# Kernel optimization log

Measured on AMD Instinct MI355X. Metric: run time of the kernel, lower is better.

The kernel has to match this reference:

```python
import jax, jax.numpy as jnp
import numpy as np

B, D, W = 2048, 512, 512
DEPTH = 6
N_BINS = 2 ** DEPTH          # 64 leaves
N_NODES = 2 ** DEPTH - 1     # 63 inner nodes


def build_indices(depth: int) -> np.ndarray:
    """Root-to-leaf path index table into hstack([probs, 1-probs]).
    Index j selects probs[:, j]; index j + N selects 1 - probs[:, j]."""
    n = 2 ** depth - 1
    paths = []
    for b in range(2 ** depth):
        node, path = 0, []
        for level in range(depth):
            bit = (b >> (depth - 1 - level)) & 1
            path.append(node if bit == 0 else node + n)
            node = 2 * node + 1 + bit
        paths.append(path)
    return np.asarray(paths, dtype=np.int32)  # [2**depth, depth]


def setup_inputs() -> dict:
    key = jax.random.key(0)
    k1, k2, k3, k4 = jax.random.split(key, 4)
    x = jax.random.normal(k1, (B, D), dtype=jnp.float32)
    ray = jax.random.normal(k2, (1, D), dtype=jnp.float32)  # kaiming-normal init
    w_i = jnp.zeros((1, N_NODES), dtype=jnp.float32)
    b_i = jax.random.normal(k3, (1, N_NODES), dtype=jnp.float32)
    a_i = 5.0 * jnp.ones((1, N_NODES), dtype=jnp.float32)
    # kaiming-normal over fan_in = input_width
    inner_transforms = jax.random.normal(k4, (N_BINS, D, W), dtype=jnp.float32) * np.float32((2.0 / D) ** 0.5)
    idx = jnp.asarray(build_indices(DEPTH))  # [64, 6] int32
    return {"x": x, "ray": ray, "w_i": w_i, "b_i": b_i, "a_i": a_i,
            "inner_transforms": inner_transforms, "idx": idx}


def reference(x, ray, w_i, b_i, a_i, inner_transforms, idx):
    eps = 1e-8
    # angles: arccos(cosine_similarity(x, ray)) / pi  -> [B]
    xn = jnp.maximum(jnp.linalg.norm(x, axis=1), eps)
    rn = jnp.maximum(jnp.linalg.norm(ray, axis=1), eps)  # [1]
    cos = (x @ ray[0]) / (xn * rn)
    angles = jnp.arccos(cos) / jnp.pi  # [B]
    # per-node decision probabilities: [B, N_NODES]
    node_fns = (0.5 + jax.nn.sigmoid(w_i)) * angles[:, None] - jax.nn.sigmoid(b_i)
    decisions = jax.nn.sigmoid(node_fns * (1.0 + a_i))
    # tree-indexed gather + product over path -> soft bin distribution [B, N_BINS]
    stacked = jnp.concatenate([decisions, 1.0 - decisions], axis=1)  # [B, 2N]
    bins, depth = idx.shape
    gathered = stacked[:, idx.reshape(-1)].reshape(x.shape[0], bins, depth)
    distribution = jnp.prod(gathered, axis=2)  # [B, L]
    # per-bin linear transforms, weighted by the distribution
    inner = jnp.einsum('bi,liw->blw', x, inner_transforms)  # [B, L, W]
    return jnp.einsum('bl,blo->bo', distribution, inner)  # [B, W]
```

## Files before the change

### kernel.cpp

```cpp
#include <hip/hip_runtime.h>
#include <math.h>

typedef float  f32x4  __attribute__((ext_vector_type(4)));
typedef float  f32x2  __attribute__((ext_vector_type(2)));
typedef short  bf16x8 __attribute__((ext_vector_type(8)));
typedef unsigned short u16x8 __attribute__((ext_vector_type(8)));
typedef unsigned short u16x4 __attribute__((ext_vector_type(4)));

#define B_ROWS 2048
#define D_DIM  512
#define W_DIM  512
#define N_NODES 63
#define N_BINS  64
#define K_TOT   32768
#define NSPLIT  8
#define LPS     (N_BINS / NSPLIT)
#define DEPS    1e-12f

__device__ __forceinline__ unsigned short f2bf(float f) {
    union { float f; unsigned int u; } v; v.f = f;
    unsigned int u = v.u;
    return (unsigned short)((u + 0x7fffu + ((u >> 16) & 1u)) >> 16);
}

__device__ __forceinline__ float sigmoidf_(float z) {
    return 1.0f / (1.0f + expf(-z));
}

__device__ __forceinline__ void load_lds16(const void* g, void* l) {
    __builtin_amdgcn_global_load_lds(
        (const __attribute__((address_space(1))) unsigned int*)g,
        (__attribute__((address_space(3))) unsigned int*)l,
        16, 0, 0);
}

__global__ __launch_bounds__(256) void k_pre(
    const float* __restrict__ x, const float* __restrict__ ray,
    const float* __restrict__ w_i, const float* __restrict__ b_i,
    const float* __restrict__ a_i, const int* __restrict__ idx,
    const float* __restrict__ T,
    float* __restrict__ dist, unsigned short* __restrict__ xb,
    unsigned short* __restrict__ Tt)
{
    __shared__ float tile[64][65];
    const int bid = blockIdx.x;
    const int t   = threadIdx.x;

    if (bid < 4096) {
        const int i0 = (bid & 7) * 64;
        const int w0 = ((bid >> 3) & 7) * 64;
        const int l  = bid >> 6;

        const int w4 = (t & 15) * 4;
        const int ir = t >> 4;
        const float* src = T + ((size_t)(l * 512 + i0)) * 512 + w0;
#pragma unroll
        for (int p = 0; p < 4; ++p) {
            int i = ir + p * 16;
            f32x4 v = *(const f32x4*)(src + (size_t)i * 512 + w4);
            tile[i][w4 + 0] = v.x; tile[i][w4 + 1] = v.y;
            tile[i][w4 + 2] = v.z; tile[i][w4 + 3] = v.w;
        }
        __syncthreads();
#pragma unroll
        for (int rep = 0; rep < 2; ++rep) {
            int id = t + rep * 256;
            int w  = id >> 3;
            int c  = id & 7;
            u16x8 o;
#pragma unroll
            for (int j = 0; j < 8; ++j) o[j] = f2bf(tile[c * 8 + j][w]);
            *(u16x8*)(Tt + (size_t)(w0 + w) * K_TOT + l * 512 + i0 + c * 8) = o;
        }
        return;
    }

    const int pb   = bid - 4096;
    const int wid  = t >> 6;
    const int lane = t & 63;
    const int row  = pb * 4 + wid;
    const float* xr = x + (size_t)row * D_DIM;

    float dotv = 0.f, xx = 0.f, rr = 0.f;
#pragma unroll
    for (int j = 0; j < 2; ++j) {
        f32x4 xv = *(const f32x4*)(xr  + j * 256 + lane * 4);
        f32x4 rv = *(const f32x4*)(ray + j * 256 + lane * 4);
        dotv += xv.x * rv.x + xv.y * rv.y + xv.z * rv.z + xv.w * rv.w;
        xx   += xv.x * xv.x + xv.y * xv.y + xv.z * xv.z + xv.w * xv.w;
        rr   += rv.x * rv.x + rv.y * rv.y + rv.z * rv.z + rv.w * rv.w;
        u16x4 o;
        o[0] = f2bf(xv.x); o[1] = f2bf(xv.y); o[2] = f2bf(xv.z); o[3] = f2bf(xv.w);
        *(u16x4*)(xb + (size_t)row * D_DIM + j * 256 + lane * 4) = o;
    }
#pragma unroll
    for (int off = 1; off < 64; off <<= 1) {
        dotv += __shfl_xor(dotv, off, 64);
        xx   += __shfl_xor(xx,   off, 64);
        rr   += __shfl_xor(rr,   off, 64);
    }
    float xn = fmaxf(sqrtf(xx), 1e-8f);
    float rn = fmaxf(sqrtf(rr), 1e-8f);
    float cosv = dotv / (xn * rn);
    cosv = fminf(1.f, fmaxf(-1.f, cosv));
    float angle = acosf(cosv) * 0.31830988618379067f;

    float dec = 0.f;
    if (lane < N_NODES) {
        float sw = sigmoidf_(w_i[lane]);
        float sb = sigmoidf_(b_i[lane]);
        float nf = (0.5f + sw) * angle - sb;
        dec = sigmoidf_(nf * (1.0f + a_i[lane]));
    }

    float p = 1.f;
#pragma unroll
    for (int v = 0; v < 6; ++v) {
        int j = idx[lane * 6 + v];
        int node = (j < N_NODES) ? j : j - N_NODES;
        float d = __shfl(dec, node, 64);
        p *= (j < N_NODES) ? d : (1.0f - d);
    }
    dist[(size_t)row * N_BINS + lane] = p;
}

__global__ __launch_bounds__(256, 2) void k_gemm9(
    const unsigned short* __restrict__ xb, const unsigned short* __restrict__ Tt,
    const float* __restrict__ dist, float* __restrict__ part)
{
    __shared__ unsigned short As[2][128 * 64];
    __shared__ unsigned short Bs[2][128 * 64];

    const int b   = blockIdx.x;
    const int xcd = b & 7;
    const int j   = b >> 3;
    const int combo = xcd * 4 + (j >> 4);
    const int mblk  = j & 15;
    const int bm0 = mblk * 128;
    const int bn0 = (combo & 3) * 128;
    const int z   = combo >> 2;
    const int l0  = z * LPS;

    const int t    = threadIdx.x;
    const int lane = t & 63;
    const int wid  = t >> 6;
    const int wm = wid >> 1, wn = wid & 1;
    const int lq = lane >> 4, lr = lane & 15;

    const int srow = t >> 3;
    const int c    = t & 7;

    f32x4 acc[4][4];
#pragma unroll
    for (int a = 0; a < 4; ++a)
#pragma unroll
        for (int bb = 0; bb < 4; ++bb)
            acc[a][bb] = (f32x4){0.f, 0.f, 0.f, 0.f};

    const int NIT = LPS * 8;

#define STAGE(it_, buf_)                                                      \
    {                                                                         \
        const int l_  = l0 + ((it_) >> 3);                                    \
        const int i0_ = ((it_) & 7) * 64;                                     \
        _Pragma("unroll")                                                     \
        for (int jj = 0; jj < 4; ++jj) {                                      \
            int row = srow + jj * 32;                                         \
            int cg_ = c ^ (row & 7);                                          \
            load_lds16(xb + (size_t)(bm0 + row) * D_DIM + i0_ + cg_ * 8,      \
                       &As[buf_][row * 64 + c * 8]);                          \
            load_lds16(Tt + (size_t)(bn0 + row) * K_TOT + (size_t)l_ * 512    \
                           + i0_ + cg_ * 8,                                   \
                       &Bs[buf_][row * 64 + c * 8]);                          \
        }                                                                     \
    }

    STAGE(0, 0);

    for (int it = 0; it < NIT; ++it) {
        __syncthreads();
        if (it + 1 < NIT) STAGE(it + 1, (it + 1) & 1);

        if ((it & 7) == 0 && it > 0) {
            const int l = l0 + (it >> 3);
#pragma unroll
            for (int fm = 0; fm < 4; ++fm)
#pragma unroll
                for (int r = 0; r < 4; ++r) {
                    int m = bm0 + wm * 64 + fm * 16 + lq * 4 + r;
                    f32x2 dd = *(const f32x2*)(dist + (size_t)m * N_BINS + (l - 1));
                    float dp = fmaxf(dd.x, DEPS);
                    float dn = fmaxf(dd.y, DEPS);
                    float ratio = dp * __builtin_amdgcn_rcpf(dn);
#pragma unroll
                    for (int fn = 0; fn < 4; ++fn)
                        acc[fm][fn][r] *= ratio;
                }
        }

        const int buf = it & 1;
#pragma unroll
        for (int ks = 0; ks < 2; ++ks) {
            bf16x8 af[4], bfr[4];
#pragma unroll
            for (int fm = 0; fm < 4; ++fm) {
                int m = wm * 64 + fm * 16 + lr;
                int g = ks * 4 + lq;
                af[fm] = *(const bf16x8*)&As[buf][m * 64 + ((g ^ (m & 7)) * 8)];
            }
#pragma unroll
            for (int fn = 0; fn < 4; ++fn) {
                int n = wn * 64 + fn * 16 + lr;
                int g = ks * 4 + lq;
                bfr[fn] = *(const bf16x8*)&Bs[buf][n * 64 + ((g ^ (n & 7)) * 8)];
            }
#pragma unroll
            for (int fm = 0; fm < 4; ++fm)
#pragma unroll
                for (int fn = 0; fn < 4; ++fn)
                    acc[fm][fn] = __builtin_amdgcn_mfma_f32_16x16x32_bf16(
                        af[fm], bfr[fn], acc[fm][fn], 0, 0, 0);
        }
    }

    float* Cp = part + (size_t)z * (B_ROWS * W_DIM);
#pragma unroll
    for (int fm = 0; fm < 4; ++fm)
#pragma unroll
        for (int r = 0; r < 4; ++r) {
            int m = bm0 + wm * 64 + fm * 16 + lq * 4 + r;
            float dl = fmaxf(dist[(size_t)m * N_BINS + (l0 + LPS - 1)], DEPS);
#pragma unroll
            for (int fn = 0; fn < 4; ++fn) {
                int col = bn0 + wn * 64 + fn * 16 + lr;
                Cp[(size_t)m * W_DIM + col] = acc[fm][fn][r] * dl;
            }
        }
#undef STAGE
}

__global__ __launch_bounds__(256) void k_reduce(
    const float* __restrict__ part, float* __restrict__ out, int nsplit)
{
    int i = (blockIdx.x * 256 + threadIdx.x) * 4;
    f32x4 s = *(const f32x4*)(part + i);
    for (int p = 1; p < nsplit; ++p)
        s += *(const f32x4*)(part + (size_t)p * (B_ROWS * W_DIM) + i);
    *(f32x4*)(out + i) = s;
}

__global__ __launch_bounds__(256, 2) void k_gemm_bt(
    const float* __restrict__ x, const float* __restrict__ dist,
    const unsigned short* __restrict__ Tt, float* __restrict__ part,
    int kchunk)
{
    __shared__ unsigned short As[128][72];
    __shared__ unsigned short Bs[128][64];

    const int bm0 = blockIdx.x * 128;
    const int bn0 = blockIdx.y * 128;
    const int kbase = blockIdx.z * kchunk;

    const int lane = threadIdx.x & 63;
    const int wid  = threadIdx.x >> 6;
    const int wm = wid >> 1, wn = wid & 1;
    const int lq = lane >> 4, lr = lane & 15;

    f32x4 acc[4][4];
#pragma unroll
    for (int a = 0; a < 4; ++a)
#pragma unroll
        for (int b = 0; b < 4; ++b)
            acc[a][b] = (f32x4){0.f, 0.f, 0.f, 0.f};

    const int iters = kchunk / 64;
    for (int it = 0; it < iters; ++it) {
        const int k0 = kbase + it * 64;
        const int l  = k0 >> 9;
        const int i0 = k0 & 511;
#pragma unroll
        for (int r2 = 0; r2 < 8; ++r2) {
            int id = threadIdx.x + r2 * 256;
            int m  = id >> 4;
            int kc = id & 15;
            float sc = dist[(size_t)(bm0 + m) * N_BINS + l];
            f32x4 v = *(const f32x4*)(x + (size_t)(bm0 + m) * D_DIM + i0 + kc * 4);
            v *= sc;
            unsigned int p0 = (unsigned int)f2bf(v.x) | ((unsigned int)f2bf(v.y) << 16);
            unsigned int p1 = (unsigned int)f2bf(v.z) | ((unsigned int)f2bf(v.w) << 16);
            unsigned int* dp = (unsigned int*)&As[m][kc * 4];
            dp[0] = p0; dp[1] = p1;
        }
#pragma unroll
        for (int r2 = 0; r2 < 4; ++r2) {
            int id = threadIdx.x + r2 * 256;
            int n  = id >> 3;
            int cc = id & 7;
            int cg = cc ^ (n & 7);
            const u16x8 v = *(const u16x8*)(Tt + (size_t)(bn0 + n) * K_TOT + k0 + cg * 8);
            *(u16x8*)&Bs[n][cc * 8] = v;
        }
        __syncthreads();
#pragma unroll
        for (int ks = 0; ks < 2; ++ks) {
            bf16x8 af[4], bfr[4];
#pragma unroll
            for (int fm = 0; fm < 4; ++fm)
                af[fm] = *(const bf16x8*)&As[wm * 64 + fm * 16 + lr][ks * 32 + lq * 8];
#pragma unroll
            for (int fn = 0; fn < 4; ++fn) {
                int nl = wn * 64 + fn * 16 + lr;
                int cs = (ks * 4 + lq) ^ (nl & 7);
                bfr[fn] = *(const bf16x8*)&Bs[nl][cs * 8];
            }
#pragma unroll
            for (int fm = 0; fm < 4; ++fm)
#pragma unroll
                for (int fn = 0; fn < 4; ++fn)
                    acc[fm][fn] = __builtin_amdgcn_mfma_f32_16x16x32_bf16(
                        af[fm], bfr[fn], acc[fm][fn], 0, 0, 0);
        }
        __syncthreads();
    }

    float* Cp = part + (size_t)blockIdx.z * (B_ROWS * W_DIM);
#pragma unroll
    for (int fm = 0; fm < 4; ++fm)
#pragma unroll
        for (int fn = 0; fn < 4; ++fn)
#pragma unroll
            for (int r = 0; r < 4; ++r) {
                int row = bm0 + wm * 64 + fm * 16 + lq * 4 + r;
                int col = bn0 + wn * 64 + fn * 16 + lr;
                Cp[(size_t)row * W_DIM + col] = acc[fm][fn][r];
            }
}

extern "C" void kernel_launch(void* const* d_in, const int* in_sizes, int n_in,
                              void* d_out, int out_size, void* d_ws, size_t ws_size,
                              hipStream_t stream) {
    const float* x   = (const float*)d_in[0];
    const float* ray = (const float*)d_in[1];
    const float* w_i = (const float*)d_in[2];
    const float* b_i = (const float*)d_in[3];
    const float* a_i = (const float*)d_in[4];
    const float* T   = (const float*)d_in[5];
    const int*   idx = (const int*)d_in[6];
    float* out = (float*)d_out;

    char* ws = (char*)d_ws;
    const size_t distBytes = (size_t)B_ROWS * N_BINS * 4;
    const size_t xbBytes   = (size_t)B_ROWS * D_DIM * 2;
    const size_t ttBytes   = (size_t)W_DIM * K_TOT * 2;
    const size_t partBytes = (size_t)B_ROWS * W_DIM * 4;

    float*          dist = (float*)ws;
    unsigned short* xb   = (unsigned short*)(ws + distBytes);
    unsigned short* Tt   = (unsigned short*)(ws + distBytes + xbBytes);

    if (ws_size >= distBytes + xbBytes + ttBytes + (size_t)NSPLIT * partBytes) {
        float* part = (float*)(ws + distBytes + xbBytes + ttBytes);

        k_pre<<<4096 + 512, 256, 0, stream>>>(x, ray, w_i, b_i, a_i, idx, T,
                                              dist, xb, Tt);
        k_gemm9<<<512, 256, 0, stream>>>(xb, Tt, dist, part);
        k_reduce<<<(B_ROWS * W_DIM) / (256 * 4), 256, 0, stream>>>(part, out, NSPLIT);
    } else if (ws_size >= distBytes + xbBytes + ttBytes) {
        k_pre<<<4096 + 512, 256, 0, stream>>>(x, ray, w_i, b_i, a_i, idx, T,
                                              dist, xb, Tt);
        k_gemm_bt<<<dim3(16, 4, 1), 256, 0, stream>>>(x, dist, Tt, out, K_TOT);
    }
}
```

Before: 192.2 us.

## Use 256x128 tiles with 512 threads and a triple-buffered async prefetch pipeline

The GEMM kernel moves from 128x128 tiles with 256 threads and a double-buffered LDS to 256x128 tiles with 512 threads and three LDS slots. The global-to-LDS loads for the tile two steps ahead are split across the two k-halves and interleaved with the MFMA work, with explicit vmcnt waits, raw s_barrier, and s_setprio around the MFMA blocks. The aim is to hide memory latency better and reuse each loaded B tile across more rows. It uses more LDS and halves the grid to 256 blocks, so occupancy and block scheduling across CUs may change.

```diff
diff --git a/kernel.cpp b/kernel.cpp
--- a/kernel.cpp
+++ b/kernel.cpp
@@ -124,22 +124,19 @@
     dist[(size_t)row * N_BINS + lane] = p;
 }
 
-__global__ __launch_bounds__(256, 2) void k_gemm9(
+__global__ __launch_bounds__(512, 2) void k_gemm10(
     const unsigned short* __restrict__ xb, const unsigned short* __restrict__ Tt,
     const float* __restrict__ dist, float* __restrict__ part)
 {
-    __shared__ unsigned short As[2][128 * 64];
-    __shared__ unsigned short Bs[2][128 * 64];
-
-    const int b   = blockIdx.x;
-    const int xcd = b & 7;
-    const int j   = b >> 3;
-    const int combo = xcd * 4 + (j >> 4);
-    const int mblk  = j & 15;
-    const int bm0 = mblk * 128;
-    const int bn0 = (combo & 3) * 128;
-    const int z   = combo >> 2;
-    const int l0  = z * LPS;
+    __shared__ unsigned short As[3][256 * 64];
+    __shared__ unsigned short Bs[3][128 * 64];
+
+    const int b    = blockIdx.x;
+    const int z    = b & 7;
+    const int tile = b >> 3;
+    const int bm0  = (tile & 7) * 256;
+    const int bn0  = (tile >> 3) * 128;
+    const int l0   = z * LPS;
 
     const int t    = threadIdx.x;
     const int lane = t & 63;
@@ -157,32 +154,38 @@
         for (int bb = 0; bb < 4; ++bb)
             acc[a][bb] = (f32x4){0.f, 0.f, 0.f, 0.f};
 
-    const int NIT = LPS * 8;
-
-#define STAGE(it_, buf_)                                                      \
+#define STAGE_A(u_, slot_, g_)                                                \
     {                                                                         \
-        const int l_  = l0 + ((it_) >> 3);                                    \
-        const int i0_ = ((it_) & 7) * 64;                                     \
-        _Pragma("unroll")                                                     \
-        for (int jj = 0; jj < 4; ++jj) {                                      \
-            int row = srow + jj * 32;                                         \
-            int cg_ = c ^ (row & 7);                                          \
-            load_lds16(xb + (size_t)(bm0 + row) * D_DIM + i0_ + cg_ * 8,      \
-                       &As[buf_][row * 64 + c * 8]);                          \
-            load_lds16(Tt + (size_t)(bn0 + row) * K_TOT + (size_t)l_ * 512    \
-                           + i0_ + cg_ * 8,                                   \
-                       &Bs[buf_][row * 64 + c * 8]);                          \
-        }                                                                     \
-    }
-
-    STAGE(0, 0);
-
-    for (int it = 0; it < NIT; ++it) {
-        __syncthreads();
-        if (it + 1 < NIT) STAGE(it + 1, (it + 1) & 1);
-
-        if ((it & 7) == 0 && it > 0) {
-            const int l = l0 + (it >> 3);
+        const int i0_  = ((u_) & 7) * 64;                                     \
+        const int row_ = srow + (g_) * 64;                                    \
+        const int cg_  = c ^ (row_ & 7);                                      \
+        load_lds16(xb + (size_t)(bm0 + row_) * D_DIM + i0_ + cg_ * 8,         \
+                   &As[slot_][row_ * 64 + c * 8]);                            \
+    }
+#define STAGE_B(u_, slot_, g_)                                                \
+    {                                                                         \
+        const int l_   = l0 + ((u_) >> 3);                                    \
+        const int i0_  = ((u_) & 7) * 64;                                     \
+        const int row_ = srow + (g_) * 64;                                    \
+        const int cg_  = c ^ (row_ & 7);                                      \
+        load_lds16(Tt + (size_t)(bn0 + row_) * K_TOT + (size_t)l_ * 512       \
+                       + i0_ + cg_ * 8,                                       \
+                   &Bs[slot_][row_ * 64 + c * 8]);                            \
+    }
+
+    STAGE_A(0, 0, 0) STAGE_A(0, 0, 1) STAGE_A(0, 0, 2) STAGE_A(0, 0, 3)
+    STAGE_B(0, 0, 0) STAGE_B(0, 0, 1)
+    STAGE_A(1, 1, 0) STAGE_A(1, 1, 1) STAGE_A(1, 1, 2) STAGE_A(1, 1, 3)
+    STAGE_B(1, 1, 0) STAGE_B(1, 1, 1)
+
+    int rs = 0;
+    for (int u = 0; u < 64; ++u) {
+        if (u < 63) asm volatile("s_waitcnt vmcnt(6)" ::: "memory");
+        else        asm volatile("s_waitcnt vmcnt(0)" ::: "memory");
+        __builtin_amdgcn_s_barrier();
+
+        if ((u & 7) == 0 && u > 0) {
+            const int l = l0 + (u >> 3);
 #pragma unroll
             for (int fm = 0; fm < 4; ++fm)
 #pragma unroll
@@ -198,30 +201,59 @@
                 }
         }
 
-        const int buf = it & 1;
-#pragma unroll
-        for (int ks = 0; ks < 2; ++ks) {
-            bf16x8 af[4], bfr[4];
+        const int ws_ = (rs == 0) ? 2 : rs - 1;
+        const bool pf = (u + 2 < 64);
+
+        {
+            bf16x8 af[4], bfv[4];
 #pragma unroll
             for (int fm = 0; fm < 4; ++fm) {
                 int m = wm * 64 + fm * 16 + lr;
-                int g = ks * 4 + lq;
-                af[fm] = *(const bf16x8*)&As[buf][m * 64 + ((g ^ (m & 7)) * 8)];
+                af[fm] = *(const bf16x8*)&As[rs][m * 64 + ((lq ^ (m & 7)) * 8)];
             }
 #pragma unroll
             for (int fn = 0; fn < 4; ++fn) {
                 int n = wn * 64 + fn * 16 + lr;
-                int g = ks * 4 + lq;
-                bfr[fn] = *(const bf16x8*)&Bs[buf][n * 64 + ((g ^ (n & 7)) * 8)];
-            }
+                bfv[fn] = *(const bf16x8*)&Bs[rs][n * 64 + ((lq ^ (n & 7)) * 8)];
+            }
+            if (pf) { STAGE_A(u + 2, ws_, 0) STAGE_A(u + 2, ws_, 1) STAGE_A(u + 2, ws_, 2) }
+            __builtin_amdgcn_s_setprio(1);
 #pragma unroll
             for (int fm = 0; fm < 4; ++fm)
 #pragma unroll
                 for (int fn = 0; fn < 4; ++fn)
                     acc[fm][fn] = __builtin_amdgcn_mfma_f32_16x16x32_bf16(
-                        af[fm], bfr[fn], acc[fm][fn], 0, 0, 0);
-        }
-    }
+                        af[fm], bfv[fn], acc[fm][fn], 0, 0, 0);
+            __builtin_amdgcn_s_setprio(0);
+        }
+        __builtin_amdgcn_s_barrier();
+        {
+            bf16x8 af[4], bfv[4];
+#pragma unroll
+            for (int fm = 0; fm < 4; ++fm) {
+                int m = wm * 64 + fm * 16 + lr;
+                af[fm] = *(const bf16x8*)&As[rs][m * 64 + (((4 + lq) ^ (m & 7)) * 8)];
+            }
+#pragma unroll
+            for (int fn = 0; fn < 4; ++fn) {
+                int n = wn * 64 + fn * 16 + lr;
+                bfv[fn] = *(const bf16x8*)&Bs[rs][n * 64 + (((4 + lq) ^ (n & 7)) * 8)];
+            }
+            if (pf) { STAGE_A(u + 2, ws_, 3) STAGE_B(u + 2, ws_, 0) STAGE_B(u + 2, ws_, 1) }
+            __builtin_amdgcn_s_setprio(1);
+#pragma unroll
+            for (int fm = 0; fm < 4; ++fm)
+#pragma unroll
+                for (int fn = 0; fn < 4; ++fn)
+                    acc[fm][fn] = __builtin_amdgcn_mfma_f32_16x16x32_bf16(
+                        af[fm], bfv[fn], acc[fm][fn], 0, 0, 0);
+            __builtin_amdgcn_s_setprio(0);
+        }
+
+        rs = (rs == 2) ? 0 : rs + 1;
+    }
+#undef STAGE_A
+#undef STAGE_B
 
     float* Cp = part + (size_t)z * (B_ROWS * W_DIM);
 #pragma unroll
@@ -236,7 +268,6 @@
                 Cp[(size_t)m * W_DIM + col] = acc[fm][fn][r] * dl;
             }
         }
-#undef STAGE
 }
 
 __global__ __launch_bounds__(256) void k_reduce(
@@ -363,7 +394,7 @@
 
         k_pre<<<4096 + 512, 256, 0, stream>>>(x, ray, w_i, b_i, a_i, idx, T,
                                               dist, xb, Tt);
-        k_gemm9<<<512, 256, 0, stream>>>(xb, Tt, dist, part);
+        k_gemm10<<<256, 512, 0, stream>>>(xb, Tt, dist, part);
         k_reduce<<<(B_ROWS * W_DIM) / (256 * 4), 256, 0, stream>>>(part, out, NSPLIT);
     } else if (ws_size >= distBytes + xbBytes + ttBytes) {
         k_pre<<<4096 + 512, 256, 0, stream>>>(x, ray, w_i, b_i, a_i, idx, T,
```

Measured after the change: 187.5 us. 1.03x faster.
